# Kernel tuning notes

Measured on AMD Instinct MI355X. Metric: run time of the kernel, lower is better.

## Reference

```python
import jax, jax.numpy as jnp
import numpy as np

B, S, D = 2, 2048, 1024
H = 16
HD = D // H  # 64


def _rope_tables(seq_len, head_dim, dtype=jnp.float32):
    inv_freq = 1.0 / (10000.0 ** (jnp.arange(0, head_dim, 2, dtype=jnp.float32) / head_dim))
    t = jnp.arange(seq_len, dtype=jnp.float32)
    freqs = jnp.einsum('i,j->ij', t, inv_freq)            # [S, HD/2]
    emb = jnp.concatenate([freqs, freqs], axis=-1)        # [S, HD]
    return jnp.cos(emb).astype(dtype)[None, None], jnp.sin(emb).astype(dtype)[None, None]


def _rotate_half(x):
    x1, x2 = x[..., : x.shape[-1] // 2], x[..., x.shape[-1] // 2 :]
    return jnp.concatenate([-x2, x1], axis=-1)


def setup_inputs() -> dict:
    key = jax.random.key(0)
    ks = jax.random.split(key, 9)
    s = 0.02
    return {
        'hidden_states': jax.random.normal(ks[0], (B, S, D), jnp.float32),
        'attention_mask': jnp.zeros((B, 1, S, S), jnp.float32),
        'Wq': jax.random.normal(ks[1], (D, D), jnp.float32) * s,
        'bq': jnp.zeros((D,), jnp.float32),
        'Wk': jax.random.normal(ks[2], (D, D), jnp.float32) * s,
        'bk': jnp.zeros((D,), jnp.float32),
        'Wv': jax.random.normal(ks[3], (D, D), jnp.float32) * s,
        'bv': jnp.zeros((D,), jnp.float32),
        'Wo': jax.random.normal(ks[4], (D, D), jnp.float32) * s,
        'bo': jnp.zeros((D,), jnp.float32),
    }


def reference(hidden_states, attention_mask, Wq, bq, Wk, bk, Wv, bv, Wo, bo):
    b, s = hidden_states.shape[:2]
    q = hidden_states @ Wq.T + bq
    k = hidden_states @ Wk.T + bk
    v = hidden_states @ Wv.T + bv
    # [B, H, S, HD]
    q = q.reshape(b, s, H, HD).transpose(0, 2, 1, 3)
    k = k.reshape(b, s, H, HD).transpose(0, 2, 1, 3)
    v = v.reshape(b, s, H, HD).transpose(0, 2, 1, 3)
    cos, sin = _rope_tables(s, HD, q.dtype)
    q = q * cos + _rotate_half(q) * sin
    k = k * cos + _rotate_half(k) * sin
    scaling = HD ** (-0.5)
    scores = jnp.einsum('bhqd,bhkd->bhqk', q, k) * scaling
    scores = scores / jnp.log(jnp.asarray(float(s), scores.dtype))  # dynamic NTK
    scores = scores + attention_mask
    probs = jax.nn.softmax(scores, axis=-1)
    out = jnp.einsum('bhqk,bhkd->bhqd', probs, v)
    out = out.transpose(0, 2, 1, 3).reshape(b, s, H * HD)
    return out @ Wo.T + bo
```

## Files before the change

### kernel.cpp

```cpp
#include <hip/hip_runtime.h>
#include <math.h>

#define S_LEN 2048
#define NHEAD 16
#define HDIM  64

typedef __attribute__((ext_vector_type(8))) short bf16x8;
typedef __attribute__((ext_vector_type(4))) float f32x4;

__device__ __forceinline__ unsigned short f2bf(float f) {
    union { float f; unsigned u; } v; v.f = f;
    unsigned r = v.u + 0x7fffu + ((v.u >> 16) & 1u);
    return (unsigned short)(r >> 16);
}

__device__ __forceinline__ void gl2lds16(const void* g, void* l) {
    __builtin_amdgcn_global_load_lds(
        (__attribute__((address_space(1))) void*)(void*)(g),
        (__attribute__((address_space(3))) void*)(l), 16, 0, 0);
}

__global__ __launch_bounds__(256) void convert_kernel(
    const float* __restrict__ hs, const float* __restrict__ Wq,
    const float* __restrict__ Wk, const float* __restrict__ Wv,
    const float* __restrict__ Wo, unsigned short* __restrict__ dst)
{
    const int gid = blockIdx.x * 256 + threadIdx.x;
    const int n = gid << 2;
    const float* src; int off;
    if (n < (4 << 20))      { src = hs; off = n; }
    else if (n < (5 << 20)) { src = Wq; off = n - (4 << 20); }
    else if (n < (6 << 20)) { src = Wk; off = n - (5 << 20); }
    else if (n < (7 << 20)) { src = Wv; off = n - (6 << 20); }
    else                    { src = Wo; off = n - (7 << 20); }
    const float4 v = *(const float4*)(src + off);
    ushort4 o;
    o.x = f2bf(v.x); o.y = f2bf(v.y); o.z = f2bf(v.z); o.w = f2bf(v.w);
    *(ushort4*)(dst + n) = o;
}

__global__ __launch_bounds__(256, 3) void qkv_gemm_kernel(
    const unsigned short* __restrict__ X,
    const unsigned short* __restrict__ Wall,
    const float* __restrict__ bq, const float* __restrict__ bk,
    const float* __restrict__ bv,
    unsigned short* __restrict__ qo, unsigned short* __restrict__ ko,
    unsigned short* __restrict__ vo)
{
    __shared__ unsigned short As[128 * 64];
    __shared__ unsigned short Bs[128 * 64];

    const int mat = blockIdx.x >> 3;
    const int n0  = (blockIdx.x & 7) << 7;
    const int m0  = blockIdx.y << 7;
    const unsigned short* W = Wall + (mat << 20);
    const float* bias = (mat == 0) ? bq : (mat == 1) ? bk : bv;
    unsigned short* out = (mat == 0) ? qo : (mat == 1) ? ko : vo;

    const int tid = threadIdx.x;
    const int wave = tid >> 6, lane = tid & 63;
    const int quad = lane >> 4, ln = lane & 15;
    const int wm = (wave >> 1) << 6, wn = (wave & 1) << 6;

    f32x4 acc[4][4] = {};

    for (int k0 = 0; k0 < 1024; k0 += 64) {
        #pragma unroll
        for (int L = 0; L < 4; ++L) {
            const int i = tid + (L << 8);
            const int r = i >> 3, cl = i & 7;
            const int cg = (cl ^ (r & 7)) << 3;
            gl2lds16(X + (m0 + r) * 1024 + k0 + cg, &As[i << 3]);
            gl2lds16(W + (n0 + r) * 1024 + k0 + cg, &Bs[i << 3]);
        }
        __syncthreads();
        #pragma unroll
        for (int s = 0; s < 2; ++s) {
            bf16x8 a[4], b[4];
            #pragma unroll
            for (int t = 0; t < 4; ++t) {
                const int ra = wm + (t << 4) + ln;
                a[t] = *(const bf16x8*)&As[(ra << 6) + ((((s << 2) | quad) ^ (ra & 7)) << 3)];
                const int rb = wn + (t << 4) + ln;
                b[t] = *(const bf16x8*)&Bs[(rb << 6) + ((((s << 2) | quad) ^ (rb & 7)) << 3)];
            }
            #pragma unroll
            for (int i = 0; i < 4; ++i)
                #pragma unroll
                for (int j = 0; j < 4; ++j)
                    acc[i][j] = __builtin_amdgcn_mfma_f32_16x16x32_bf16(a[i], b[j], acc[i][j], 0, 0, 0);
        }
        __syncthreads();
    }

    float bv4[4];
    #pragma unroll
    for (int jt = 0; jt < 4; ++jt) bv4[jt] = bias[n0 + wn + (jt << 4) + ln];

    const float l2c = 0.41524101186092029f;
    const int h = (n0 + wn) >> 6;

    #pragma unroll
    for (int i = 0; i < 4; ++i) {
        #pragma unroll
        for (int reg = 0; reg < 4; ++reg) {
            const int m = m0 + wm + (i << 4) + (quad << 2) + reg;
            const int b_ = m >> 11, s_ = m & 2047;
            unsigned short* o = out + ((((b_ << 4) + h) << 11) + s_) * 64;
            if (mat < 2) {
                #pragma unroll
                for (int jl = 0; jl < 2; ++jl) {
                    const int hd = (jl << 4) + ln;
                    const float ang = (float)s_ * exp2f(-(float)hd * l2c);
                    float c, sn; sincosf(ang, &sn, &c);
                    const float x1 = acc[i][jl][reg] + bv4[jl];
                    const float x2 = acc[i][jl + 2][reg] + bv4[jl + 2];
                    o[hd]      = f2bf(x1 * c - x2 * sn);
                    o[hd + 32] = f2bf(x2 * c + x1 * sn);
                }
            } else {
                #pragma unroll
                for (int jt = 0; jt < 4; ++jt) {
                    const int hd = (jt << 4) + ln;
                    o[hd] = f2bf(acc[i][jt][reg] + bv4[jt]);
                }
            }
        }
    }
}

__global__ __launch_bounds__(256) void vtrans_kernel(
    const unsigned short* __restrict__ v, unsigned short* __restrict__ vt)
{
    __shared__ unsigned short T[64][66];
    const int bh = blockIdx.x >> 5;
    const int s0 = (blockIdx.x & 31) << 6;
    const int tid = threadIdx.x;
    #pragma unroll
    for (int L = 0; L < 4; ++L) {
        const int i = tid + (L << 8);
        const int r = i >> 4, c4 = (i & 15) << 2;
        const ushort4 in = *(const ushort4*)(v + ((bh << 11) + s0 + r) * 64 + c4);
        T[r][c4 + 0] = in.x; T[r][c4 + 1] = in.y;
        T[r][c4 + 2] = in.z; T[r][c4 + 3] = in.w;
    }
    __syncthreads();
    #pragma unroll
    for (int L = 0; L < 4; ++L) {
        const int i = tid + (L << 8);
        const int hd = i >> 4, c4 = (i & 15) << 2;
        ushort4 o;
        o.x = T[c4 + 0][hd]; o.y = T[c4 + 1][hd];
        o.z = T[c4 + 2][hd]; o.w = T[c4 + 3][hd];
        *(ushort4*)(vt + ((bh << 6) + hd) * 2048 + s0 + c4) = o;
    }
}

__global__ __launch_bounds__(256, 4) void flash_kernel(
    const unsigned short* __restrict__ qb, const unsigned short* __restrict__ kb,
    const unsigned short* __restrict__ vtb, const float* __restrict__ mask,
    unsigned short* __restrict__ attn)
{
    __shared__ unsigned short Ks[2][64 * 64];
    __shared__ unsigned short Vt[2][64 * 64];
    __shared__ unsigned short Ps[64 * 64];

    const int qt = blockIdx.x & 31;
    const int bh = blockIdx.x >> 5;
    const int b_ = bh >> 4, h = bh & 15;
    const int q0 = qt << 6;

    const int tid = threadIdx.x;
    const int wave = tid >> 6, lane = tid & 63;
    const int quad = lane >> 4, ln = lane & 15;

    const unsigned short* qrow = qb + ((size_t)((bh << 11) + q0 + (wave << 4) + ln) << 6);
    bf16x8 qa[2];
    qa[0] = *(const bf16x8*)(qrow + (quad << 3));
    qa[1] = *(const bf16x8*)(qrow + 32 + (quad << 3));

    const float LOG2E = 1.4426950408889634f;
    const float scale2 = (0.125f / logf(2048.0f)) * LOG2E;

    const float* mbase = mask + ((size_t)b_ << 22)
                       + ((size_t)(q0 + (wave << 4) + (quad << 2)) << 11) + ln;

    unsigned short* Pw = Ps + (wave << 10);

    float l_i[4] = {0.f, 0.f, 0.f, 0.f};
    f32x4 O[4] = {};

    #pragma unroll
    for (int L = 0; L < 2; ++L) {
        const int i = tid + (L << 8);
        const int r = i >> 3, cl = i & 7;
        const int cg = (cl ^ (r & 7)) << 3;
        gl2lds16(kb + ((bh << 11) + r) * 64 + cg, &Ks[0][i << 3]);
        gl2lds16(vtb + ((bh << 6) + r) * 2048 + cg, &Vt[0][i << 3]);
    }
    float mcur[4][4];
    #pragma unroll
    for (int reg = 0; reg < 4; ++reg)
        #pragma unroll
        for (int j = 0; j < 4; ++j)
            mcur[reg][j] = mbase[(reg << 11) + (j << 4)] * LOG2E;

    for (int kt = 0; kt < 32; ++kt) {
        const int cur = kt & 1;

        __syncthreads();

        float mnext[4][4];
        if (kt < 31) {
            const int kn = (kt + 1) << 6;
            #pragma unroll
            for (int L = 0; L < 2; ++L) {
                const int i = tid + (L << 8);
                const int r = i >> 3, cl = i & 7;
                const int cg = (cl ^ (r & 7)) << 3;
                gl2lds16(kb + ((bh << 11) + kn + r) * 64 + cg, &Ks[cur ^ 1][i << 3]);
                gl2lds16(vtb + ((bh << 6) + r) * 2048 + kn + cg, &Vt[cur ^ 1][i << 3]);
            }
            #pragma unroll
            for (int reg = 0; reg < 4; ++reg)
                #pragma unroll
                for (int j = 0; j < 4; ++j)
                    mnext[reg][j] = mbase[(reg << 11) + kn + (j << 4)] * LOG2E;
        }

        f32x4 sacc[4] = {};
        #pragma unroll
        for (int s = 0; s < 2; ++s) {
            bf16x8 bfr[4];
            #pragma unroll
            for (int j = 0; j < 4; ++j) {
                const int r = (j << 4) + ln;
                bfr[j] = *(const bf16x8*)&Ks[cur][(r << 6) + ((((s << 2) | quad) ^ (r & 7)) << 3)];
            }
            #pragma unroll
            for (int j = 0; j < 4; ++j)
                sacc[j] = __builtin_amdgcn_mfma_f32_16x16x32_bf16(qa[s], bfr[j], sacc[j], 0, 0, 0);
        }

        #pragma unroll
        for (int reg = 0; reg < 4; ++reg) {
            const int pr = (quad << 2) + reg;
            #pragma unroll
            for (int j = 0; j < 4; ++j) {
                const float p = exp2f(fmaf(sacc[j][reg], scale2, mcur[reg][j]));
                l_i[reg] += p;
                const int c = (j << 4) + ln;
                Pw[(pr << 6) + (((c >> 3) ^ (pr & 7)) << 3) + (c & 7)] = f2bf(p);
            }
        }

        #pragma unroll
        for (int s = 0; s < 2; ++s) {
            const bf16x8 a = *(const bf16x8*)&Pw[(ln << 6) + ((((s << 2) | quad) ^ (ln & 7)) << 3)];
            bf16x8 bfr[4];
            #pragma unroll
            for (int j = 0; j < 4; ++j) {
                const int r = (j << 4) + ln;
                bfr[j] = *(const bf16x8*)&Vt[cur][(r << 6) + ((((s << 2) | quad) ^ (r & 7)) << 3)];
            }
            #pragma unroll
            for (int j = 0; j < 4; ++j)
                O[j] = __builtin_amdgcn_mfma_f32_16x16x32_bf16(a, bfr[j], O[j], 0, 0, 0);
        }

        if (kt < 31) {
            #pragma unroll
            for (int reg = 0; reg < 4; ++reg)
                #pragma unroll
                for (int j = 0; j < 4; ++j)
                    mcur[reg][j] = mnext[reg][j];
        }
    }

    #pragma unroll
    for (int reg = 0; reg < 4; ++reg) {
        float l = l_i[reg];
        l += __shfl_xor(l, 1);
        l += __shfl_xor(l, 2);
        l += __shfl_xor(l, 4);
        l += __shfl_xor(l, 8);
        const float inv = 1.0f / l;
        const int qr = q0 + (wave << 4) + (quad << 2) + reg;
        unsigned short* op = attn + (((size_t)((b_ << 11) + qr)) << 10) + (h << 6);
        #pragma unroll
        for (int j = 0; j < 4; ++j)
            op[(j << 4) + ln] = f2bf(O[j][reg] * inv);
    }
}

__global__ __launch_bounds__(256, 3) void out_gemm_kernel(
    const unsigned short* __restrict__ X, const unsigned short* __restrict__ W,
    const float* __restrict__ bias, float* __restrict__ out)
{
    __shared__ unsigned short As[128 * 64];
    __shared__ unsigned short Bs[128 * 64];

    const int n0 = blockIdx.x << 7;
    const int m0 = blockIdx.y << 7;
    const int tid = threadIdx.x;
    const int wave = tid >> 6, lane = tid & 63;
    const int quad = lane >> 4, ln = lane & 15;
    const int wm = (wave >> 1) << 6, wn = (wave & 1) << 6;

    f32x4 acc[4][4] = {};

    for (int k0 = 0; k0 < 1024; k0 += 64) {
        #pragma unroll
        for (int L = 0; L < 4; ++L) {
            const int i = tid + (L << 8);
            const int r = i >> 3, cl = i & 7;
            const int cg = (cl ^ (r & 7)) << 3;
            gl2lds16(X + (m0 + r) * 1024 + k0 + cg, &As[i << 3]);
            gl2lds16(W + (n0 + r) * 1024 + k0 + cg, &Bs[i << 3]);
        }
        __syncthreads();
        #pragma unroll
        for (int s = 0; s < 2; ++s) {
            bf16x8 a[4], b[4];
            #pragma unroll
            for (int t = 0; t < 4; ++t) {
                const int ra = wm + (t << 4) + ln;
                a[t] = *(const bf16x8*)&As[(ra << 6) + ((((s << 2) | quad) ^ (ra & 7)) << 3)];
                const int rb = wn + (t << 4) + ln;
                b[t] = *(const bf16x8*)&Bs[(rb << 6) + ((((s << 2) | quad) ^ (rb & 7)) << 3)];
            }
            #pragma unroll
            for (int i = 0; i < 4; ++i)
                #pragma unroll
                for (int j = 0; j < 4; ++j)
                    acc[i][j] = __builtin_amdgcn_mfma_f32_16x16x32_bf16(a[i], b[j], acc[i][j], 0, 0, 0);
        }
        __syncthreads();
    }

    float bv4[4];
    #pragma unroll
    for (int jt = 0; jt < 4; ++jt) bv4[jt] = bias[n0 + wn + (jt << 4) + ln];

    #pragma unroll
    for (int i = 0; i < 4; ++i)
        #pragma unroll
        for (int reg = 0; reg < 4; ++reg) {
            const int m = m0 + wm + (i << 4) + (quad << 2) + reg;
            #pragma unroll
            for (int jt = 0; jt < 4; ++jt) {
                const int n = n0 + wn + (jt << 4) + ln;
                out[m * 1024 + n] = acc[i][jt][reg] + bv4[jt];
            }
        }
}

extern "C" void kernel_launch(void* const* d_in, const int* in_sizes, int n_in,
                              void* d_out, int out_size, void* d_ws, size_t ws_size,
                              hipStream_t stream)
{
    const float* hs   = (const float*)d_in[0];
    const float* mask = (const float*)d_in[1];
    const float* Wq   = (const float*)d_in[2];
    const float* bq   = (const float*)d_in[3];
    const float* Wk   = (const float*)d_in[4];
    const float* bk   = (const float*)d_in[5];
    const float* Wv   = (const float*)d_in[6];
    const float* bv   = (const float*)d_in[7];
    const float* Wo   = (const float*)d_in[8];
    const float* bo   = (const float*)d_in[9];

    unsigned short* ws = (unsigned short*)d_ws;
    const size_t M1 = (size_t)1 << 20;
    unsigned short* hsb   = ws;
    unsigned short* wall  = ws + 4 * M1;
    unsigned short* wob   = ws + 7 * M1;
    unsigned short* qbf   = ws + 8 * M1;
    unsigned short* kbf   = ws + 12 * M1;
    unsigned short* vbf   = ws + 16 * M1;
    unsigned short* vtb   = ws + 20 * M1;
    unsigned short* attnb = ws + 24 * M1;

    convert_kernel<<<8192, 256, 0, stream>>>(hs, Wq, Wk, Wv, Wo, ws);
    qkv_gemm_kernel<<<dim3(24, 32), 256, 0, stream>>>(hsb, wall, bq, bk, bv, qbf, kbf, vbf);
    vtrans_kernel<<<1024, 256, 0, stream>>>(vbf, vtb);
    flash_kernel<<<1024, 256, 0, stream>>>(qbf, kbf, vtb, mask, attnb);
    out_gemm_kernel<<<dim3(8, 32), 256, 0, stream>>>(attnb, wob, bo, (float*)d_out);
}
```

Measured before the change: 250.8 us.

## Permute key order to vectorize P stores, precompute RoPE table, use fast exp

```diff
diff --git a/kernel.cpp b/kernel.cpp
--- a/kernel.cpp
+++ b/kernel.cpp
@@ -18,6 +18,19 @@
     __builtin_amdgcn_global_load_lds(
         (__attribute__((address_space(1))) void*)(void*)(g),
         (__attribute__((address_space(3))) void*)(l), 16, 0, 0);
+}
+
+__global__ __launch_bounds__(256) void rope_tab_kernel(float2* __restrict__ tab)
+{
+    const int gid = blockIdx.x * 256 + threadIdx.x;
+    const int s = gid >> 5, i = gid & 31;
+    const float l2c = 0.41524101186092029f;
+    const float freq = exp2f(-(float)i * l2c);
+    const float ang = (float)s * freq;
+    float2 cs;
+    cs.x = cosf(ang);
+    cs.y = sinf(ang);
+    tab[gid] = cs;
 }
 
 __global__ __launch_bounds__(256) void convert_kernel(
@@ -43,7 +56,7 @@
     const unsigned short* __restrict__ X,
     const unsigned short* __restrict__ Wall,
     const float* __restrict__ bq, const float* __restrict__ bk,
-    const float* __restrict__ bv,
+    const float* __restrict__ bv, const float2* __restrict__ rtab,
     unsigned short* __restrict__ qo, unsigned short* __restrict__ ko,
     unsigned short* __restrict__ vo)
 {
@@ -97,7 +110,6 @@
     #pragma unroll
     for (int jt = 0; jt < 4; ++jt) bv4[jt] = bias[n0 + wn + (jt << 4) + ln];
 
-    const float l2c = 0.41524101186092029f;
     const int h = (n0 + wn) >> 6;
 
     #pragma unroll
@@ -111,12 +123,11 @@
                 #pragma unroll
                 for (int jl = 0; jl < 2; ++jl) {
                     const int hd = (jl << 4) + ln;
-                    const float ang = (float)s_ * exp2f(-(float)hd * l2c);
-                    float c, sn; sincosf(ang, &sn, &c);
+                    const float2 cs = rtab[(s_ << 5) + hd];
                     const float x1 = acc[i][jl][reg] + bv4[jl];
                     const float x2 = acc[i][jl + 2][reg] + bv4[jl + 2];
-                    o[hd]      = f2bf(x1 * c - x2 * sn);
-                    o[hd + 32] = f2bf(x2 * c + x1 * sn);
+                    o[hd]      = f2bf(x1 * cs.x - x2 * cs.y);
+                    o[hd + 32] = f2bf(x2 * cs.x + x1 * cs.y);
                 }
             } else {
                 #pragma unroll
@@ -148,11 +159,11 @@
     #pragma unroll
     for (int L = 0; L < 4; ++L) {
         const int i = tid + (L << 8);
-        const int hd = i >> 4, c4 = (i & 15) << 2;
+        const int hd = i >> 4, b = i & 15;
         ushort4 o;
-        o.x = T[c4 + 0][hd]; o.y = T[c4 + 1][hd];
-        o.z = T[c4 + 2][hd]; o.w = T[c4 + 3][hd];
-        *(ushort4*)(vt + ((bh << 6) + hd) * 2048 + s0 + c4) = o;
+        o.x = T[b][hd];      o.y = T[b + 16][hd];
+        o.z = T[b + 32][hd]; o.w = T[b + 48][hd];
+        *(ushort4*)(vt + ((bh << 6) + hd) * 2048 + s0 + (b << 2)) = o;
     }
 }
 
@@ -179,8 +190,7 @@
     qa[0] = *(const bf16x8*)(qrow + (quad << 3));
     qa[1] = *(const bf16x8*)(qrow + 32 + (quad << 3));
 
-    const float LOG2E = 1.4426950408889634f;
-    const float scale2 = (0.125f / logf(2048.0f)) * LOG2E;
+    const float scale = 0.125f / logf(2048.0f);
 
     const float* mbase = mask + ((size_t)b_ << 22)
                        + ((size_t)(q0 + (wave << 4) + (quad << 2)) << 11) + ln;
@@ -203,7 +213,7 @@
     for (int reg = 0; reg < 4; ++reg)
         #pragma unroll
         for (int j = 0; j < 4; ++j)
-            mcur[reg][j] = mbase[(reg << 11) + (j << 4)] * LOG2E;
+            mcur[reg][j] = mbase[(reg << 11) + (j << 4)];
 
     for (int kt = 0; kt < 32; ++kt) {
         const int cur = kt & 1;
@@ -225,7 +235,7 @@
             for (int reg = 0; reg < 4; ++reg)
                 #pragma unroll
                 for (int j = 0; j < 4; ++j)
-                    mnext[reg][j] = mbase[(reg << 11) + kn + (j << 4)] * LOG2E;
+                    mnext[reg][j] = mbase[(reg << 11) + kn + (j << 4)];
         }
 
         f32x4 sacc[4] = {};
@@ -245,13 +255,21 @@
         #pragma unroll
         for (int reg = 0; reg < 4; ++reg) {
             const int pr = (quad << 2) + reg;
+            float p[4];
             #pragma unroll
             for (int j = 0; j < 4; ++j) {
-                const float p = exp2f(fmaf(sacc[j][reg], scale2, mcur[reg][j]));
-                l_i[reg] += p;
-                const int c = (j << 4) + ln;
-                Pw[(pr << 6) + (((c >> 3) ^ (pr & 7)) << 3) + (c & 7)] = f2bf(p);
-            }
+                p[j] = __expf(fmaf(sacc[j][reg], scale, mcur[reg][j]));
+                l_i[reg] += p[j];
+            }
+            unsigned u0 = __float_as_uint(p[0]) + 0x8000u;
+            unsigned u1 = __float_as_uint(p[1]) + 0x8000u;
+            unsigned u2 = __float_as_uint(p[2]) + 0x8000u;
+            unsigned u3 = __float_as_uint(p[3]) + 0x8000u;
+            uint2 w;
+            w.x = __builtin_amdgcn_perm(u1, u0, 0x07060302u);
+            w.y = __builtin_amdgcn_perm(u3, u2, 0x07060302u);
+            const int e = (pr << 6) + ((((ln >> 1) ^ (pr & 7)) << 3)) + ((ln & 1) << 2);
+            *(uint2*)&Pw[e] = w;
         }
 
         #pragma unroll
@@ -380,9 +398,11 @@
     unsigned short* vbf   = ws + 16 * M1;
     unsigned short* vtb   = ws + 20 * M1;
     unsigned short* attnb = ws + 24 * M1;
-
+    float2*         rtab  = (float2*)(ws + 28 * M1);
+
+    rope_tab_kernel<<<256, 256, 0, stream>>>(rtab);
     convert_kernel<<<8192, 256, 0, stream>>>(hs, Wq, Wk, Wv, Wo, ws);
-    qkv_gemm_kernel<<<dim3(24, 32), 256, 0, stream>>>(hsb, wall, bq, bk, bv, qbf, kbf, vbf);
+    qkv_gemm_kernel<<<dim3(24, 32), 256, 0, stream>>>(hsb, wall, bq, bk, bv, rtab, qbf, kbf, vbf);
     vtrans_kernel<<<1024, 256, 0, stream>>>(vbf, vtb);
     flash_kernel<<<1024, 256, 0, stream>>>(qbf, kbf, vtb, mask, attnb);
     out_gemm_kernel<<<dim3(8, 32), 256, 0, stream>>>(attnb, wob, bo, (float*)d_out);
```

Result: faster. 242.7 us (-3.2%).
